# Kernel tuning notes

Measured on AMD Instinct MI355X. Metric: run time of the kernel, lower is better.

The kernel has to match this reference:

```python
import jax, jax.numpy as jnp
import numpy as np

D_MODEL = 1024
NUM_HEADS = 16
DK = D_MODEL // NUM_HEADS
THETA = 10000.0
B, S = 4, 2048


def _rope(x, pos):
    # x: [B, H, S, dk], pos: [S] int positions
    half = DK // 2
    inv_freq = THETA ** (-jnp.arange(half, dtype=jnp.float32) * 2.0 / DK)  # [half]
    ang = pos.astype(jnp.float32)[:, None] * inv_freq[None, :]             # [S, half]
    cos, sin = jnp.cos(ang), jnp.sin(ang)                                  # [S, half]
    x_even = x[..., 0::2]
    x_odd = x[..., 1::2]
    out_even = x_even * cos - x_odd * sin
    out_odd = x_even * sin + x_odd * cos
    # interleave back to [..., dk]
    return jnp.stack([out_even, out_odd], axis=-1).reshape(x.shape)


def setup_inputs() -> dict:
    key = jax.random.key(0)
    ks = jax.random.split(key, 5)
    scale = 1.0 / np.sqrt(D_MODEL)
    return {
        "x": jax.random.normal(ks[0], (B, S, D_MODEL), dtype=jnp.float32),
        "token_position": jnp.arange(S, dtype=jnp.int32),
        "wq": jax.random.normal(ks[1], (D_MODEL, D_MODEL), dtype=jnp.float32) * scale,
        "wk": jax.random.normal(ks[2], (D_MODEL, D_MODEL), dtype=jnp.float32) * scale,
        "wv": jax.random.normal(ks[3], (D_MODEL, D_MODEL), dtype=jnp.float32) * scale,
        "wo": jax.random.normal(ks[4], (D_MODEL, D_MODEL), dtype=jnp.float32) * scale,
    }


def reference(x, token_position, wq, wk, wv, wo):
    b, s, _ = x.shape
    # QKV projections (torch Linear: y = x @ W.T), split heads -> [B, H, S, dk]
    def proj(w):
        y = jnp.einsum("bsd,ed->bse", x, w)
        return y.reshape(b, s, NUM_HEADS, DK).transpose(0, 2, 1, 3)
    q, k, v = proj(wq), proj(wk), proj(wv)
    q = _rope(q, token_position)
    k = _rope(k, token_position)
    # causal SDPA
    scores = jnp.einsum("bhqd,bhkd->bhqk", q, k) / jnp.sqrt(jnp.float32(DK))
    causal = jnp.tril(jnp.ones((s, s), dtype=bool))
    scores = jnp.where(causal, scores, -jnp.inf)
    attn = jax.nn.softmax(scores, axis=-1)
    out = jnp.einsum("bhqk,bhkd->bhqd", attn, v)          # [B, H, S, dv]
    out = out.transpose(0, 2, 1, 3).reshape(b, s, D_MODEL)  # merge heads
    return jnp.einsum("bsd,ed->bse", out, wo)             # output projection
```

## Files before the change

### kernel.cpp

```cpp
#include <hip/hip_runtime.h>


#define D_MODEL 1024
#define NH      16
#define DKH     64
#define SEQ     2048
#define BATCH   4
#define M_ROWS  (BATCH * SEQ)
#define SCALE_LOG2 0.180336875461f
#define ROPE_L2    0.41524101186092029f

typedef _Float16 f16;
typedef _Float16 f16x8 __attribute__((ext_vector_type(8)));
typedef _Float16 f16x4 __attribute__((ext_vector_type(4)));
typedef _Float16 f16x2 __attribute__((ext_vector_type(2)));
typedef __fp16   fp16x2n __attribute__((ext_vector_type(2)));
typedef float    f32x4 __attribute__((ext_vector_type(4)));
typedef unsigned short u16;
typedef unsigned int   u32;

__device__ __forceinline__ void glds16(const void* g, void* l) {
  __builtin_amdgcn_global_load_lds((const __attribute__((address_space(1))) void*)g,
                                   (__attribute__((address_space(3))) void*)l, 16, 0, 0);
}
__device__ __forceinline__ u32 pk(float a, float b) {
  union { fp16x2n h; u32 u; } c; c.h = __builtin_amdgcn_cvt_pkrtz(a, b); return c.u;
}

__global__ void cvt_all(const float* __restrict__ x,
                        const float* __restrict__ w0, const float* __restrict__ w1,
                        const float* __restrict__ w2, const float* __restrict__ w3,
                        f16* __restrict__ xo, f16* __restrict__ o0, f16* __restrict__ o1,
                        f16* __restrict__ o2, f16* __restrict__ o3) {
  int blk = blockIdx.x;
  const float* src; f16* dst; int off;
  if (blk < 8192) { src = x; dst = xo; off = blk; }
  else {
    int t = blk - 8192; int w = t >> 10; off = t & 1023;
    switch (w) { case 0: src = w0; dst = o0; break;  case 1: src = w1; dst = o1; break;
                 case 2: src = w2; dst = o2; break;  default: src = w3; dst = o3; break; }
  }
  int i = (off * 256 + threadIdx.x) * 4;
  float4 v = *(const float4*)(src + i);
  uint2 o; o.x = pk(v.x, v.y); o.y = pk(v.z, v.w);
  *(uint2*)(dst + i) = o;
}

template<int MODE>
__global__ __launch_bounds__(256) void gemm_glds(const f16* __restrict__ A,
                                                 const f16* __restrict__ W,
                                                 void* __restrict__ C0,
                                                 void* __restrict__ C1,
                                                 void* __restrict__ C2,
                                                 const int* __restrict__ pos,
                                                 int K) {
  __shared__ f16 As[128][64];
  __shared__ f16 Bs[128][64];
  const int tid  = threadIdx.x;
  const int m0   = blockIdx.y * 128;
  const int n0   = blockIdx.x * 128;
  const int wave = tid >> 6, lane = tid & 63;
  const int quad = lane >> 4, l16 = lane & 15;
  const int wm = (wave >> 1) * 64, wn = (wave & 1) * 64;

  f32x4 acc[4][4];
#pragma unroll
  for (int i = 0; i < 4; ++i)
#pragma unroll
    for (int j = 0; j < 4; ++j) acc[i][j] = (f32x4){0.f, 0.f, 0.f, 0.f};

  for (int k0 = 0; k0 < K; k0 += 64) {
    if (k0) __syncthreads();
#pragma unroll
    for (int i = 0; i < 4; ++i) {
      int ci  = i * 256 + tid;
      int row = ci >> 3, ch = ci & 7;
      glds16(A + (size_t)(m0 + row) * K + k0 + ch * 8,
             (char*)&As[0][0] + (size_t)(i * 256 + (tid & 192)) * 16);
      glds16(W + (size_t)(n0 + row) * K + k0 + ch * 8,
             (char*)&Bs[0][0] + (size_t)(i * 256 + (tid & 192)) * 16);
    }
    __syncthreads();
#pragma unroll
    for (int kk = 0; kk < 64; kk += 32) {
      f16x8 af[4], bfr[4];
#pragma unroll
      for (int mi = 0; mi < 4; ++mi)
        af[mi] = *(const f16x8*)&As[wm + mi * 16 + l16][kk + quad * 8];
#pragma unroll
      for (int ni = 0; ni < 4; ++ni)
        bfr[ni] = *(const f16x8*)&Bs[wn + ni * 16 + l16][kk + quad * 8];
#pragma unroll
      for (int mi = 0; mi < 4; ++mi)
#pragma unroll
        for (int ni = 0; ni < 4; ++ni)
          acc[mi][ni] = __builtin_amdgcn_mfma_f32_16x16x32_f16(af[mi], bfr[ni], acc[mi][ni], 0, 0, 0);
    }
  }

  if (MODE == 1) {
    f16* dst; int nb;
    if (n0 < 1024)      { dst = (f16*)C0; nb = n0; }
    else if (n0 < 2048) { dst = (f16*)C1; nb = n0 - 1024; }
    else                { dst = (f16*)C2; nb = n0 - 2048; }
    if (n0 < 2048) {
      float invf[4], sgn[4];
#pragma unroll
      for (int ni = 0; ni < 4; ++ni) {
        int dk = (wn + ni * 16 + l16) & 63;
        invf[ni] = __builtin_amdgcn_exp2f(-ROPE_L2 * (float)(dk >> 1));
        sgn[ni]  = (dk & 1) ? 1.f : -1.f;
      }
#pragma unroll
      for (int mi = 0; mi < 4; ++mi)
#pragma unroll
        for (int r = 0; r < 4; ++r) {
          int row = m0 + wm + mi * 16 + quad * 4 + r;
          float ps = (float)pos[row & (SEQ - 1)];
#pragma unroll
          for (int ni = 0; ni < 4; ++ni) {
            float ang = ps * invf[ni];
            float c = __cosf(ang), sn = __sinf(ang);
            float v = acc[mi][ni][r];
            float p = __shfl_xor(v, 1);
            float ov = fmaf(p * sgn[ni], sn, v * c);
            int col = nb + wn + ni * 16 + l16;
            dst[(size_t)row * 1024 + col] = (f16)ov;
          }
        }
    } else {
#pragma unroll
      for (int mi = 0; mi < 4; ++mi)
#pragma unroll
        for (int ni = 0; ni < 4; ++ni)
#pragma unroll
          for (int r = 0; r < 4; ++r) {
            int row = m0 + wm + mi * 16 + quad * 4 + r;
            int col = nb + wn + ni * 16 + l16;
            dst[(size_t)row * 1024 + col] = (f16)acc[mi][ni][r];
          }
    }
  } else {
    float* dst = (float*)C0;
#pragma unroll
    for (int mi = 0; mi < 4; ++mi)
#pragma unroll
      for (int ni = 0; ni < 4; ++ni)
#pragma unroll
        for (int r = 0; r < 4; ++r) {
          int row = m0 + wm + mi * 16 + quad * 4 + r;
          int col = n0 + wn + ni * 16 + l16;
          dst[(size_t)row * 1024 + col] = acc[mi][ni][r];
        }
  }
}

__global__ __launch_bounds__(256, 3) void flash_attn(const f16* __restrict__ Q,
                                                     const f16* __restrict__ Kg,
                                                     const f16* __restrict__ Vg,
                                                     f16* __restrict__ O) {
  __shared__ char smem[38400];
  f16*  KsL         = (f16*)smem;
  u32   (*Vt)[67]   = (u32(*)[67])(smem + 16384);
  float (*Red0)[66] = (float(*)[66])smem;
  float (*Red1)[66] = (float(*)[66])(smem + 16896);
  float (*Lb)[17]   = (float(*)[17])(smem + 33792);

  const int tid  = threadIdx.x;
  const int bh   = blockIdx.x;
  const int b    = bh >> 4, h = bh & 15;
  const int qblk = 31 - (int)blockIdx.y;
  const int q0   = qblk * 64;
  const int wave = tid >> 6, lane = tid & 63;
  const int quad = lane >> 4, l16 = lane & 15;
  const int nkt  = (qblk + 2) >> 1;

  f16x8 qf[4][2];
#pragma unroll
  for (int nt = 0; nt < 4; ++nt)
#pragma unroll
    for (int ks = 0; ks < 2; ++ks) {
      f16x8 qv = *(const f16x8*)(Q + ((size_t)(b * SEQ + q0 + nt * 16 + l16)) * D_MODEL
                                   + h * DKH + ks * 32 + quad * 8);
      qf[nt][ks] = qv * (f16)SCALE_LOG2;
    }

  f32x4 o[4][4];
#pragma unroll
  for (int md = 0; md < 4; ++md)
#pragma unroll
    for (int nt = 0; nt < 4; ++nt) o[md][nt] = (f32x4){0.f, 0.f, 0.f, 0.f};
  float lacc[4] = {0.f, 0.f, 0.f, 0.f};

  const int kp = tid >> 3, dc = (tid & 7) * 8;

  for (int t = 0; t < nkt; ++t) {
    const int kt = t * 128;
    const f16* vb = Vg + ((size_t)(b * SEQ + kt + 2 * kp)) * D_MODEL + h * DKH + dc;
    uint4 v0 = *(const uint4*)vb;
    uint4 v1 = *(const uint4*)(vb + D_MODEL);
    uint4 v2 = *(const uint4*)(vb + 64 * D_MODEL);
    uint4 v3 = *(const uint4*)(vb + 65 * D_MODEL);

    if (t) __syncthreads();
#pragma unroll
    for (int i = 0; i < 4; ++i) {
      int ci = i * 256 + tid;
      int row = ci >> 3, gc = (ci & 7) ^ (row & 7);
      glds16(Kg + ((size_t)(b * SEQ + kt + row)) * D_MODEL + h * DKH + gc * 8,
             smem + (size_t)(i * 256 + (tid & 192)) * 16);
    }
    {
      union { uint4 u; u16 s[8]; } a0, a1, a2, a3;
      a0.u = v0; a1.u = v1; a2.u = v2; a3.u = v3;
#pragma unroll
      for (int j = 0; j < 8; ++j) {
        Vt[dc + j][kp]      = (u32)a0.s[j] | ((u32)a1.s[j] << 16);
        Vt[dc + j][32 + kp] = (u32)a2.s[j] | ((u32)a3.s[j] << 16);
      }
    }
    __syncthreads();

    f16x4 pb[2][4];
#pragma unroll
    for (int mt = 0; mt < 2; ++mt) {
      const int krow = wave * 32 + mt * 16 + l16;
      const int s0 = quad ^ (krow & 7);
      f16x8 ka0 = *(const f16x8*)(KsL + krow * 64 + s0 * 8);
      f16x8 ka1 = *(const f16x8*)(KsL + krow * 64 + (s0 ^ 4) * 8);
      const int keyb = kt + wave * 32 + mt * 16 + quad * 4;
#pragma unroll
      for (int nt = 0; nt < 4; ++nt) {
        f32x4 c = (f32x4){0.f, 0.f, 0.f, 0.f};
        c = __builtin_amdgcn_mfma_f32_16x16x32_f16(ka0, qf[nt][0], c, 0, 0, 0);
        c = __builtin_amdgcn_mfma_f32_16x16x32_f16(ka1, qf[nt][1], c, 0, 0, 0);
        const int q = q0 + nt * 16 + l16;
        float p0 = __builtin_amdgcn_exp2f(c[0]);
        float p1 = __builtin_amdgcn_exp2f(c[1]);
        float p2 = __builtin_amdgcn_exp2f(c[2]);
        float p3 = __builtin_amdgcn_exp2f(c[3]);
        if (t == nkt - 1) {
          p0 = (keyb + 0 <= q) ? p0 : 0.f;
          p1 = (keyb + 1 <= q) ? p1 : 0.f;
          p2 = (keyb + 2 <= q) ? p2 : 0.f;
          p3 = (keyb + 3 <= q) ? p3 : 0.f;
        }
        lacc[nt] += (p0 + p1) + (p2 + p3);
        union { u32 w[2]; f16x4 v; } pp;
        pp.w[0] = pk(p0, p1); pp.w[1] = pk(p2, p3);
        pb[mt][nt] = pp.v;
      }
    }

#pragma unroll
    for (int md = 0; md < 4; ++md)
#pragma unroll
      for (int ks2 = 0; ks2 < 2; ++ks2) {
        const u32* vp = &Vt[md * 16 + l16][wave * 16 + ks2 * 8 + quad * 2];
        union { u32 x[2]; f16x4 v; } va;
        va.x[0] = vp[0]; va.x[1] = vp[1];
#pragma unroll
        for (int nt = 0; nt < 4; ++nt)
          o[md][nt] = __builtin_amdgcn_mfma_f32_16x16x16f16(va.v, pb[ks2][nt], o[md][nt], 0, 0, 0);
      }
  }

  __syncthreads();
  {
    float (*Rw)[66] = (wave >= 2) ? Red1 : Red0;
    if ((wave & 1) == 0) {
#pragma unroll
      for (int md = 0; md < 4; ++md)
#pragma unroll
        for (int nt = 0; nt < 4; ++nt)
#pragma unroll
          for (int r = 0; r < 4; ++r)
            Rw[md * 16 + quad * 4 + r][nt * 16 + l16] = o[md][nt][r];
    }
#pragma unroll
    for (int nt = 0; nt < 4; ++nt)
      Lb[nt * 16 + l16][wave * 4 + quad] = lacc[nt];
    __syncthreads();
    if (wave & 1) {
#pragma unroll
      for (int md = 0; md < 4; ++md)
#pragma unroll
        for (int nt = 0; nt < 4; ++nt)
#pragma unroll
          for (int r = 0; r < 4; ++r)
            Rw[md * 16 + quad * 4 + r][nt * 16 + l16] += o[md][nt][r];
    }
    __syncthreads();
  }

  {
    const int q = tid & 63, dc4 = (tid >> 6) * 16;
    float lsum = 0.f;
#pragma unroll
    for (int j = 0; j < 16; ++j) lsum += Lb[q][j];
    float linv = __builtin_amdgcn_rcpf(lsum);
    union { uint4 u[2]; u32 w[8]; } ov;
#pragma unroll
    for (int i = 0; i < 8; ++i) {
      float f0 = Red0[dc4 + 2 * i][q]     + Red1[dc4 + 2 * i][q];
      float f1 = Red0[dc4 + 2 * i + 1][q] + Red1[dc4 + 2 * i + 1][q];
      ov.w[i] = pk(f0 * linv, f1 * linv);
    }
    f16* op = O + ((size_t)(b * SEQ + q0 + q)) * D_MODEL + h * DKH + dc4;
    *(uint4*)op = ov.u[0];
    *(uint4*)(op + 8) = ov.u[1];
  }
}

extern "C" void kernel_launch(void* const* d_in, const int* in_sizes, int n_in,
                              void* d_out, int out_size, void* d_ws, size_t ws_size,
                              hipStream_t stream) {
  const float* x      = (const float*)d_in[0];
  const int*   tokpos = (const int*)d_in[1];
  const float* wq     = (const float*)d_in[2];
  const float* wk     = (const float*)d_in[3];
  const float* wv     = (const float*)d_in[4];
  const float* wo     = (const float*)d_in[5];
  float* out = (float*)d_out;

  char* ws = (char*)d_ws;
  f16* Xb  = (f16*)(ws + 0);
  f16* Wqb = (f16*)(ws + 16777216);
  f16* Wkb = (f16*)(ws + 18874368);
  f16* Wvb = (f16*)(ws + 20971520);
  f16* Wob = (f16*)(ws + 23068672);
  f16* Qb  = (f16*)(ws + 25165824);
  f16* Kb  = (f16*)(ws + 41943040);
  f16* Vb  = (f16*)(ws + 58720256);
  f16* Ob  = Xb;

  cvt_all<<<12288, 256, 0, stream>>>(x, wq, wk, wv, wo, Xb, Wqb, Wkb, Wvb, Wob);

  gemm_glds<1><<<dim3(24, 64), 256, 0, stream>>>(Xb, Wqb, Qb, Kb, Vb, tokpos, D_MODEL);

  flash_attn<<<dim3(BATCH * NH, 32), 256, 0, stream>>>(Qb, Kb, Vb, Ob);

  gemm_glds<0><<<dim3(8, 64), 256, 0, stream>>>(Ob, Wob, out, nullptr, nullptr, nullptr, D_MODEL);
}
```

Measured before the change: 255.9 us.

## Double-buffer GEMM with 8-wave 128x256 tiles and swizzled LDS

Replaces the single-buffered 128x128 GEMM with a 512-thread, 128x256-tile kernel. It double-buffers half-K slabs in dynamic LDS using async global-to-LDS loads and explicit vmcnt waits. It also XOR-swizzles the LDS layout to avoid bank conflicts and raises MFMA priority with setprio. The aim is to overlap global loads with MFMA work and improve operand reuse. The cost is 96KB of LDS per block and fewer blocks in the grid, which may limit occupancy and load balance on the small output projection GEMM.

```diff
diff --git a/kernel.cpp b/kernel.cpp
--- a/kernel.cpp
+++ b/kernel.cpp
@@ -13,7 +13,6 @@
 typedef _Float16 f16;
 typedef _Float16 f16x8 __attribute__((ext_vector_type(8)));
 typedef _Float16 f16x4 __attribute__((ext_vector_type(4)));
-typedef _Float16 f16x2 __attribute__((ext_vector_type(2)));
 typedef __fp16   fp16x2n __attribute__((ext_vector_type(2)));
 typedef float    f32x4 __attribute__((ext_vector_type(4)));
 typedef unsigned short u16;
@@ -46,22 +45,32 @@
   *(uint2*)(dst + i) = o;
 }
 
+__device__ __forceinline__ void mfma16(f32x4 (&acc)[4][4], const f16x8 (&af)[4],
+                                       const f16x8 (&bf)[4]) {
+#pragma unroll
+  for (int mi = 0; mi < 4; ++mi)
+#pragma unroll
+    for (int ni = 0; ni < 4; ++ni)
+      acc[mi][ni] = __builtin_amdgcn_mfma_f32_16x16x32_f16(af[mi], bf[ni], acc[mi][ni], 0, 0, 0);
+}
+
 template<int MODE>
-__global__ __launch_bounds__(256) void gemm_glds(const f16* __restrict__ A,
+__global__ __launch_bounds__(512, 2) void gemm8p(const f16* __restrict__ A,
                                                  const f16* __restrict__ W,
                                                  void* __restrict__ C0,
                                                  void* __restrict__ C1,
                                                  void* __restrict__ C2,
                                                  const int* __restrict__ pos,
                                                  int K) {
-  __shared__ f16 As[128][64];
-  __shared__ f16 Bs[128][64];
+  extern __shared__ char lds[];
   const int tid  = threadIdx.x;
   const int m0   = blockIdx.y * 128;
-  const int n0   = blockIdx.x * 128;
+  const int n0   = blockIdx.x * 256;
   const int wave = tid >> 6, lane = tid & 63;
   const int quad = lane >> 4, l16 = lane & 15;
-  const int wm = (wave >> 1) * 64, wn = (wave & 1) * 64;
+  const int wm = (wave >> 2) * 64;
+  const int wn = (wave & 3) * 64;
+  const int nt = K >> 6;
 
   f32x4 acc[4][4];
 #pragma unroll
@@ -69,32 +78,75 @@
 #pragma unroll
     for (int j = 0; j < 4; ++j) acc[i][j] = (f32x4){0.f, 0.f, 0.f, 0.f};
 
-  for (int k0 = 0; k0 < K; k0 += 64) {
-    if (k0) __syncthreads();
-#pragma unroll
-    for (int i = 0; i < 4; ++i) {
-      int ci  = i * 256 + tid;
-      int row = ci >> 3, ch = ci & 7;
-      glds16(A + (size_t)(m0 + row) * K + k0 + ch * 8,
-             (char*)&As[0][0] + (size_t)(i * 256 + (tid & 192)) * 16);
-      glds16(W + (size_t)(n0 + row) * K + k0 + ch * 8,
-             (char*)&Bs[0][0] + (size_t)(i * 256 + (tid & 192)) * 16);
-    }
-    __syncthreads();
-#pragma unroll
-    for (int kk = 0; kk < 64; kk += 32) {
-      f16x8 af[4], bfr[4];
-#pragma unroll
-      for (int mi = 0; mi < 4; ++mi)
-        af[mi] = *(const f16x8*)&As[wm + mi * 16 + l16][kk + quad * 8];
-#pragma unroll
-      for (int ni = 0; ni < 4; ++ni)
-        bfr[ni] = *(const f16x8*)&Bs[wn + ni * 16 + l16][kk + quad * 8];
-#pragma unroll
-      for (int mi = 0; mi < 4; ++mi)
-#pragma unroll
-        for (int ni = 0; ni < 4; ++ni)
-          acc[mi][ni] = __builtin_amdgcn_mfma_f32_16x16x32_f16(af[mi], bfr[ni], acc[mi][ni], 0, 0, 0);
+  auto stageA = [&](int t, int h) {
+    char* dst = lds + ((t & 1) * 16384 + h * 8192) + (size_t)(tid & 448) * 16;
+    int r = tid >> 2, c = tid & 3;
+    int g = c ^ ((r >> 1) & 3);
+    glds16(A + (size_t)(m0 + r) * K + (t * 64 + h * 32) + g * 8, dst);
+  };
+  auto stageB = [&](int t, int h) {
+    char* base = lds + 32768 + ((t & 1) * 32768 + h * 16384);
+#pragma unroll
+    for (int j = 0; j < 2; ++j) {
+      int ci = j * 512 + tid;
+      int r = ci >> 2, c = ci & 3;
+      int g = c ^ ((r >> 1) & 3);
+      glds16(W + (size_t)(n0 + r) * K + (t * 64 + h * 32) + g * 8,
+             base + (size_t)(j * 512 + (tid & 448)) * 16);
+    }
+  };
+  auto readA = [&](int t, int h, int mi) -> f16x8 {
+    int r = wm + mi * 16 + l16;
+    int c = quad ^ ((r >> 1) & 3);
+    return *(const f16x8*)(lds + (t & 1) * 16384 + h * 8192 + r * 64 + c * 16);
+  };
+  auto readB = [&](int t, int h, int ni) -> f16x8 {
+    int r = wn + ni * 16 + l16;
+    int c = quad ^ ((r >> 1) & 3);
+    return *(const f16x8*)(lds + 32768 + (t & 1) * 32768 + h * 16384 + r * 64 + c * 16);
+  };
+
+  stageA(0, 0); stageB(0, 0);
+  stageA(0, 1); stageB(0, 1);
+  stageA(1, 0); stageB(1, 0);
+  asm volatile("s_waitcnt vmcnt(6)" ::: "memory");
+  __builtin_amdgcn_sched_barrier(0);
+  __builtin_amdgcn_s_barrier();
+
+  for (int t = 0; t < nt; ++t) {
+    {
+      f16x8 af[4], bf[4];
+#pragma unroll
+      for (int i = 0; i < 4; ++i) { af[i] = readA(t, 0, i); bf[i] = readB(t, 0, i); }
+      if (t + 1 < nt) { stageA(t + 1, 1); stageB(t + 1, 1); }
+      __builtin_amdgcn_s_barrier();
+      asm volatile("s_waitcnt lgkmcnt(0)" ::: "memory");
+      __builtin_amdgcn_sched_barrier(0);
+      __builtin_amdgcn_s_setprio(1);
+      mfma16(acc, af, bf);
+      __builtin_amdgcn_s_setprio(0);
+      if (t < nt - 1) asm volatile("s_waitcnt vmcnt(6)" ::: "memory");
+      else            asm volatile("s_waitcnt vmcnt(0)" ::: "memory");
+      __builtin_amdgcn_sched_barrier(0);
+      __builtin_amdgcn_s_barrier();
+    }
+    {
+      f16x8 af[4], bf[4];
+#pragma unroll
+      for (int i = 0; i < 4; ++i) { af[i] = readA(t, 1, i); bf[i] = readB(t, 1, i); }
+      if (t + 2 < nt) { stageA(t + 2, 0); stageB(t + 2, 0); }
+      __builtin_amdgcn_s_barrier();
+      asm volatile("s_waitcnt lgkmcnt(0)" ::: "memory");
+      __builtin_amdgcn_sched_barrier(0);
+      __builtin_amdgcn_s_setprio(1);
+      mfma16(acc, af, bf);
+      __builtin_amdgcn_s_setprio(0);
+      if (t < nt - 1) {
+        if (t < nt - 2) asm volatile("s_waitcnt vmcnt(6)" ::: "memory");
+        else            asm volatile("s_waitcnt vmcnt(3)" ::: "memory");
+        __builtin_amdgcn_sched_barrier(0);
+        __builtin_amdgcn_s_barrier();
+      }
     }
   }
 
@@ -334,11 +386,22 @@
   f16* Vb  = (f16*)(ws + 58720256);
   f16* Ob  = Xb;
 
+  static bool attr_done = false;
+  if (!attr_done) {
+    auto* f1 = gemm8p<1>;
+    auto* f0 = gemm8p<0>;
+    (void)hipFuncSetAttribute(reinterpret_cast<const void*>(f1),
+                              hipFuncAttributeMaxDynamicSharedMemorySize, 98304);
+    (void)hipFuncSetAttribute(reinterpret_cast<const void*>(f0),
+                              hipFuncAttributeMaxDynamicSharedMemorySize, 98304);
+    attr_done = true;
+  }
+
   cvt_all<<<12288, 256, 0, stream>>>(x, wq, wk, wv, wo, Xb, Wqb, Wkb, Wvb, Wob);
 
-  gemm_glds<1><<<dim3(24, 64), 256, 0, stream>>>(Xb, Wqb, Qb, Kb, Vb, tokpos, D_MODEL);
+  gemm8p<1><<<dim3(12, 64), 512, 98304, stream>>>(Xb, Wqb, Qb, Kb, Vb, tokpos, D_MODEL);
 
   flash_attn<<<dim3(BATCH * NH, 32), 256, 0, stream>>>(Qb, Kb, Vb, Ob);
 
-  gemm_glds<0><<<dim3(8, 64), 256, 0, stream>>>(Ob, Wob, out, nullptr, nullptr, nullptr, D_MODEL);
-}
+  gemm8p<0><<<dim3(4, 64), 512, 98304, stream>>>(Ob, Wob, out, nullptr, nullptr, nullptr, D_MODEL);
+}
```

Measured after the change: 265.4 us. 1.04x slower.

## Rewrite projection GEMMs as 8-wave 128x256 tiles with triple-buffered LDS pipeline

Applied to the files above, without the earlier changes.

Replaces the 4-wave 128x128 GEMM with a 512-thread kernel that computes 128x256 tiles. It uses three LDS stages in 147KB of dynamic shared memory, with XOR-swizzled LDS addressing and global-to-LDS loads issued one stage ahead of the MFMA work. It also uses explicit vmcnt waits, barriers and setprio around the MFMA block to overlap memory traffic with compute. The aim is to hide global load latency and cut LDS bank conflicts in the QKV and output projections. The cost is higher LDS use, which limits occupancy to one block per CU, and a K loop hard-wired to 1024.

```diff
diff --git a/kernel.cpp b/kernel.cpp
--- a/kernel.cpp
+++ b/kernel.cpp
@@ -13,7 +13,6 @@
 typedef _Float16 f16;
 typedef _Float16 f16x8 __attribute__((ext_vector_type(8)));
 typedef _Float16 f16x4 __attribute__((ext_vector_type(4)));
-typedef _Float16 f16x2 __attribute__((ext_vector_type(2)));
 typedef __fp16   fp16x2n __attribute__((ext_vector_type(2)));
 typedef float    f32x4 __attribute__((ext_vector_type(4)));
 typedef unsigned short u16;
@@ -47,21 +46,20 @@
 }
 
 template<int MODE>
-__global__ __launch_bounds__(256) void gemm_glds(const f16* __restrict__ A,
+__global__ __launch_bounds__(512, 2) void gemm8p(const f16* __restrict__ A,
                                                  const f16* __restrict__ W,
                                                  void* __restrict__ C0,
                                                  void* __restrict__ C1,
                                                  void* __restrict__ C2,
-                                                 const int* __restrict__ pos,
-                                                 int K) {
-  __shared__ f16 As[128][64];
-  __shared__ f16 Bs[128][64];
+                                                 const int* __restrict__ pos) {
+  extern __shared__ char lds[];
   const int tid  = threadIdx.x;
   const int m0   = blockIdx.y * 128;
-  const int n0   = blockIdx.x * 128;
+  const int n0   = blockIdx.x * 256;
   const int wave = tid >> 6, lane = tid & 63;
   const int quad = lane >> 4, l16 = lane & 15;
-  const int wm = (wave >> 1) * 64, wn = (wave & 1) * 64;
+  const int wm = (wave >> 2) * 64;
+  const int wn = (wave & 3) * 64;
 
   f32x4 acc[4][4];
 #pragma unroll
@@ -69,34 +67,80 @@
 #pragma unroll
     for (int j = 0; j < 4; ++j) acc[i][j] = (f32x4){0.f, 0.f, 0.f, 0.f};
 
-  for (int k0 = 0; k0 < K; k0 += 64) {
-    if (k0) __syncthreads();
-#pragma unroll
-    for (int i = 0; i < 4; ++i) {
-      int ci  = i * 256 + tid;
-      int row = ci >> 3, ch = ci & 7;
-      glds16(A + (size_t)(m0 + row) * K + k0 + ch * 8,
-             (char*)&As[0][0] + (size_t)(i * 256 + (tid & 192)) * 16);
-      glds16(W + (size_t)(n0 + row) * K + k0 + ch * 8,
-             (char*)&Bs[0][0] + (size_t)(i * 256 + (tid & 192)) * 16);
-    }
-    __syncthreads();
-#pragma unroll
-    for (int kk = 0; kk < 64; kk += 32) {
-      f16x8 af[4], bfr[4];
-#pragma unroll
-      for (int mi = 0; mi < 4; ++mi)
-        af[mi] = *(const f16x8*)&As[wm + mi * 16 + l16][kk + quad * 8];
-#pragma unroll
-      for (int ni = 0; ni < 4; ++ni)
-        bfr[ni] = *(const f16x8*)&Bs[wn + ni * 16 + l16][kk + quad * 8];
-#pragma unroll
-      for (int mi = 0; mi < 4; ++mi)
-#pragma unroll
-        for (int ni = 0; ni < 4; ++ni)
-          acc[mi][ni] = __builtin_amdgcn_mfma_f32_16x16x32_f16(af[mi], bfr[ni], acc[mi][ni], 0, 0, 0);
-    }
-  }
+  const int cswr = (quad ^ ((l16 >> 1) & 3)) * 16;
+  const char* aB  = lds + (wm + l16) * 64 + cswr;
+  const char* bB0 = lds + 49152 + (wn + l16) * 64 + cswr;
+  const char* bB1 = bB0 + 49152;
+
+  const int sr = tid >> 2;
+  const int sg = (tid & 3) ^ ((sr >> 1) & 3);
+  const char* pA = (const char*)(A + (size_t)(m0 + sr) * 1024 + sg * 8);
+  const char* pB = (const char*)(W + (size_t)(n0 + sr) * 1024 + sg * 8);
+  char* const sA = lds + (size_t)(tid & 448) * 16;
+  char* const sB = lds + 49152 + (size_t)(tid & 448) * 16;
+
+#define STAGE(SBUF) do {                                                      \
+    glds16(pA,                sA + (SBUF) * 16384);                           \
+    glds16(pA + 64,           sA + (SBUF) * 16384 + 8192);                    \
+    glds16(pB,                sB + (SBUF) * 16384);                           \
+    glds16(pB + 262144,       sB + (SBUF) * 16384 + 8192);                    \
+    glds16(pB + 64,           sB + (SBUF) * 16384 + 49152);                   \
+    glds16(pB + 262144 + 64,  sB + (SBUF) * 16384 + 49152 + 8192);            \
+    pA += 128; pB += 128;                                                     \
+  } while (0)
+
+#define GPHASE(BUF, SBUF, DOSTAGE, VMN, LASTP) do {                           \
+    f16x8 af[4][2], bf[4][2];                                                 \
+    _Pragma("unroll")                                                         \
+    for (int mi = 0; mi < 4; ++mi) {                                          \
+      af[mi][0] = *(const f16x8*)(aB + ((BUF) * 16384 + mi * 1024));          \
+      af[mi][1] = *(const f16x8*)(aB + ((BUF) * 16384 + 8192 + mi * 1024));   \
+    }                                                                         \
+    _Pragma("unroll")                                                         \
+    for (int ni = 0; ni < 4; ++ni) {                                          \
+      bf[ni][0] = *(const f16x8*)(bB0 + ((BUF) * 16384 + ni * 1024));         \
+      bf[ni][1] = *(const f16x8*)(bB1 + ((BUF) * 16384 + ni * 1024));         \
+    }                                                                         \
+    if (DOSTAGE) STAGE(SBUF);                                                 \
+    __builtin_amdgcn_s_barrier();                                             \
+    asm volatile("s_waitcnt lgkmcnt(0)" ::: "memory");                        \
+    __builtin_amdgcn_sched_barrier(0);                                        \
+    __builtin_amdgcn_s_setprio(1);                                            \
+    _Pragma("unroll")                                                         \
+    for (int h = 0; h < 2; ++h)                                               \
+      _Pragma("unroll")                                                       \
+      for (int mi = 0; mi < 4; ++mi)                                          \
+        _Pragma("unroll")                                                     \
+        for (int ni = 0; ni < 4; ++ni)                                        \
+          acc[mi][ni] = __builtin_amdgcn_mfma_f32_16x16x32_f16(af[mi][h], bf[ni][h], \
+                                                               acc[mi][ni], 0, 0, 0); \
+    __builtin_amdgcn_s_setprio(0);                                            \
+    if (!(LASTP)) {                                                           \
+      asm volatile("s_waitcnt vmcnt(" #VMN ")" ::: "memory");                 \
+      __builtin_amdgcn_sched_barrier(0);                                      \
+      __builtin_amdgcn_s_barrier();                                           \
+    }                                                                         \
+  } while (0)
+
+  STAGE(0);
+  STAGE(1);
+  asm volatile("s_waitcnt vmcnt(6)" ::: "memory");
+  __builtin_amdgcn_sched_barrier(0);
+  __builtin_amdgcn_s_barrier();
+
+#pragma unroll 1
+  for (int it = 0; it < 4; ++it) {
+    GPHASE(0, 2, 1, 6, 0);
+    GPHASE(1, 0, 1, 6, 0);
+    GPHASE(2, 1, 1, 6, 0);
+  }
+  GPHASE(0, 2, 1, 6, 0);
+  GPHASE(1, 0, 1, 6, 0);
+  GPHASE(2, 0, 0, 0, 0);
+  GPHASE(0, 0, 0, 0, 1);
+
+#undef GPHASE
+#undef STAGE
 
   if (MODE == 1) {
     f16* dst; int nb;
@@ -334,11 +378,22 @@
   f16* Vb  = (f16*)(ws + 58720256);
   f16* Ob  = Xb;
 
+  static bool attr_done = false;
+  if (!attr_done) {
+    auto* f1 = gemm8p<1>;
+    auto* f0 = gemm8p<0>;
+    (void)hipFuncSetAttribute(reinterpret_cast<const void*>(f1),
+                              hipFuncAttributeMaxDynamicSharedMemorySize, 147456);
+    (void)hipFuncSetAttribute(reinterpret_cast<const void*>(f0),
+                              hipFuncAttributeMaxDynamicSharedMemorySize, 147456);
+    attr_done = true;
+  }
+
   cvt_all<<<12288, 256, 0, stream>>>(x, wq, wk, wv, wo, Xb, Wqb, Wkb, Wvb, Wob);
 
-  gemm_glds<1><<<dim3(24, 64), 256, 0, stream>>>(Xb, Wqb, Qb, Kb, Vb, tokpos, D_MODEL);
+  gemm8p<1><<<dim3(12, 64), 512, 147456, stream>>>(Xb, Wqb, Qb, Kb, Vb, tokpos);
 
   flash_attn<<<dim3(BATCH * NH, 32), 256, 0, stream>>>(Qb, Kb, Vb, Ob);
 
-  gemm_glds<0><<<dim3(8, 64), 256, 0, stream>>>(Ob, Wob, out, nullptr, nullptr, nullptr, D_MODEL);
-}
+  gemm8p<0><<<dim3(4, 64), 512, 147456, stream>>>(Ob, Wob, out, nullptr, nullptr, nullptr);
+}
```

Result: no change. 252.5 us (-1.3%).

## Replace GEMMs with 256x256-tile double-buffered pipelined kernel with XCD-aware block mapping

Applied to the files above, without the earlier changes.

Swaps the 128x128 single-buffered GEMM for a 512-thread, 256x256-tile kernel that double-buffers A/B tiles in 128KB of dynamic LDS. Each k-step is split into half-tile stages that interleave async global->LDS loads with MFMA, using explicit vmcnt waits, barriers and setprio. It also adds a swizzled LDS layout to cut bank conflicts and remaps block IDs so neighbouring tiles share an XCD. The aim is to hide load latency and raise arithmetic intensity. The risks are fewer blocks (only 128 for the output projection), fragile hand scheduling, and hardcoded K=1024.

```diff
diff --git a/kernel.cpp b/kernel.cpp
--- a/kernel.cpp
+++ b/kernel.cpp
@@ -6,14 +6,12 @@
 #define DKH     64
 #define SEQ     2048
 #define BATCH   4
-#define M_ROWS  (BATCH * SEQ)
 #define SCALE_LOG2 0.180336875461f
 #define ROPE_L2    0.41524101186092029f
 
 typedef _Float16 f16;
 typedef _Float16 f16x8 __attribute__((ext_vector_type(8)));
 typedef _Float16 f16x4 __attribute__((ext_vector_type(4)));
-typedef _Float16 f16x2 __attribute__((ext_vector_type(2)));
 typedef __fp16   fp16x2n __attribute__((ext_vector_type(2)));
 typedef float    f32x4 __attribute__((ext_vector_type(4)));
 typedef unsigned short u16;
@@ -46,111 +44,177 @@
   *(uint2*)(dst + i) = o;
 }
 
-template<int MODE>
-__global__ __launch_bounds__(256) void gemm_glds(const f16* __restrict__ A,
-                                                 const f16* __restrict__ W,
-                                                 void* __restrict__ C0,
-                                                 void* __restrict__ C1,
-                                                 void* __restrict__ C2,
-                                                 const int* __restrict__ pos,
-                                                 int K) {
-  __shared__ f16 As[128][64];
-  __shared__ f16 Bs[128][64];
+#define VMW_(N) asm volatile("s_waitcnt vmcnt(" #N ")" ::: "memory")
+#define VMW(N) VMW_(N)
+
+template<int MODE, int CPX, int NBX>
+__global__ __launch_bounds__(512, 2) void gemm256(const f16* __restrict__ A,
+                                                  const f16* __restrict__ W,
+                                                  void* __restrict__ C0,
+                                                  void* __restrict__ C1,
+                                                  void* __restrict__ C2,
+                                                  const int* __restrict__ pos) {
+  extern __shared__ char lds[];
+  const int bid  = blockIdx.x;
+  const int lin  = (bid & 7) * CPX + (bid >> 3);
+  const int bx   = lin % NBX, by = lin / NBX;
+  const int m0   = by * 256, n0 = bx * 256;
   const int tid  = threadIdx.x;
-  const int m0   = blockIdx.y * 128;
-  const int n0   = blockIdx.x * 128;
   const int wave = tid >> 6, lane = tid & 63;
   const int quad = lane >> 4, l16 = lane & 15;
-  const int wm = (wave >> 1) * 64, wn = (wave & 1) * 64;
-
-  f32x4 acc[4][4];
-#pragma unroll
-  for (int i = 0; i < 4; ++i)
+  const int wr   = wave >> 2, wc = wave & 3;
+
+  f32x4 acc[8][4];
+#pragma unroll
+  for (int i = 0; i < 8; ++i)
 #pragma unroll
     for (int j = 0; j < 4; ++j) acc[i][j] = (f32x4){0.f, 0.f, 0.f, 0.f};
 
-  for (int k0 = 0; k0 < K; k0 += 64) {
-    if (k0) __syncthreads();
-#pragma unroll
-    for (int i = 0; i < 4; ++i) {
-      int ci  = i * 256 + tid;
-      int row = ci >> 3, ch = ci & 7;
-      glds16(A + (size_t)(m0 + row) * K + k0 + ch * 8,
-             (char*)&As[0][0] + (size_t)(i * 256 + (tid & 192)) * 16);
-      glds16(W + (size_t)(n0 + row) * K + k0 + ch * 8,
-             (char*)&Bs[0][0] + (size_t)(i * 256 + (tid & 192)) * 16);
-    }
-    __syncthreads();
-#pragma unroll
-    for (int kk = 0; kk < 64; kk += 32) {
-      f16x8 af[4], bfr[4];
-#pragma unroll
-      for (int mi = 0; mi < 4; ++mi)
-        af[mi] = *(const f16x8*)&As[wm + mi * 16 + l16][kk + quad * 8];
-#pragma unroll
-      for (int ni = 0; ni < 4; ++ni)
-        bfr[ni] = *(const f16x8*)&Bs[wn + ni * 16 + l16][kk + quad * 8];
-#pragma unroll
-      for (int mi = 0; mi < 4; ++mi)
-#pragma unroll
-        for (int ni = 0; ni < 4; ++ni)
-          acc[mi][ni] = __builtin_amdgcn_mfma_f32_16x16x32_f16(af[mi], bfr[ni], acc[mi][ni], 0, 0, 0);
-    }
-  }
+  const int posR = (l16 & 1) * 4 + (quad ^ ((l16 >> 1) & 3));
+  const char* aRd = lds + wr * 8192 + (l16 >> 1) * 128 + posR * 16;
+  const char* bRd = lds + 65536 + wc * 4096 + (l16 >> 1) * 128 + posR * 16;
+
+  const int r0 = 2 * (tid >> 3) + ((tid & 7) >> 2);
+  const int c0 = (tid & 3) ^ ((tid >> 3) & 3);
+  const f16* pA0 = A + (size_t)(m0 + r0) * 1024 + c0 * 8;
+  const f16* pA1 = pA0 + (size_t)128 * 1024;
+  const f16* pB0 = W + (size_t)(n0 + r0) * 1024 + c0 * 8;
+  const f16* pB1 = pB0 + (size_t)128 * 1024;
+  char* const sdA = lds + (size_t)(tid & 448) * 16;
+  char* const sdB = lds + 65536 + (size_t)(tid & 448) * 16;
+
+#define ST_A(TB, H) do {                                                      \
+    glds16(pA0 + (H) * 32, sdA + (TB) * 32768 + (H) * 16384);                 \
+    glds16(pA1 + (H) * 32, sdA + (TB) * 32768 + (H) * 16384 + 8192);          \
+  } while (0)
+#define ST_B(TB, H) do {                                                      \
+    glds16(pB0 + (H) * 32, sdB + (TB) * 32768 + (H) * 16384);                 \
+    glds16(pB1 + (H) * 32, sdB + (TB) * 32768 + (H) * 16384 + 8192);          \
+  } while (0)
+#define RDA(BUF, H, MG) do { _Pragma("unroll")                                \
+    for (int i_ = 0; i_ < 4; ++i_)                                            \
+      af[i_] = *(const f16x8*)(aRd + (BUF) * 32768 + (H) * 16384 +            \
+                               (MG) * 4096 + i_ * 1024);                      \
+  } while (0)
+#define RDB(BUF, H) do { _Pragma("unroll")                                    \
+    for (int j_ = 0; j_ < 4; ++j_)                                            \
+      bf[j_] = *(const f16x8*)(bRd + (BUF) * 32768 + (H) * 16384 + j_ * 1024);\
+  } while (0)
+#define MM(MG) do { _Pragma("unroll")                                         \
+    for (int i_ = 0; i_ < 4; ++i_) { _Pragma("unroll")                        \
+      for (int j_ = 0; j_ < 4; ++j_)                                          \
+        acc[(MG) * 4 + i_][j_] = __builtin_amdgcn_mfma_f32_16x16x32_f16(      \
+            af[i_], bf[j_], acc[(MG) * 4 + i_][j_], 0, 0, 0); }               \
+  } while (0)
+#define PRE_MFMA() do {                                                       \
+    __builtin_amdgcn_s_barrier();                                             \
+    asm volatile("s_waitcnt lgkmcnt(0)" ::: "memory");                        \
+    __builtin_amdgcn_sched_barrier(0);                                        \
+  } while (0)
+
+#define TILE(BUF, DOSTAGE, VM2, VM4, LAST) do {                               \
+    f16x8 af[4], bf[4];                                                       \
+    RDA(BUF, 0, 0); RDB(BUF, 0);                                              \
+    if (DOSTAGE) ST_A((BUF) ^ 1, 0);                                          \
+    PRE_MFMA();                                                               \
+    __builtin_amdgcn_s_setprio(1); MM(0); __builtin_amdgcn_s_setprio(0);      \
+    __builtin_amdgcn_s_barrier();                                             \
+    RDA(BUF, 0, 1);                                                           \
+    if (DOSTAGE) ST_B((BUF) ^ 1, 0);                                          \
+    PRE_MFMA();                                                               \
+    __builtin_amdgcn_s_setprio(1); MM(1); __builtin_amdgcn_s_setprio(0);      \
+    VMW(VM2); __builtin_amdgcn_sched_barrier(0);                              \
+    __builtin_amdgcn_s_barrier();                                             \
+    RDA(BUF, 1, 0); RDB(BUF, 1);                                              \
+    if (DOSTAGE) ST_A((BUF) ^ 1, 1);                                          \
+    PRE_MFMA();                                                               \
+    __builtin_amdgcn_s_setprio(1); MM(0); __builtin_amdgcn_s_setprio(0);      \
+    __builtin_amdgcn_s_barrier();                                             \
+    RDA(BUF, 1, 1);                                                           \
+    if (DOSTAGE) ST_B((BUF) ^ 1, 1);                                          \
+    PRE_MFMA();                                                               \
+    __builtin_amdgcn_s_setprio(1); MM(1); __builtin_amdgcn_s_setprio(0);      \
+    if (!(LAST)) {                                                            \
+      VMW(VM4); __builtin_amdgcn_sched_barrier(0);                            \
+      __builtin_amdgcn_s_barrier();                                           \
+    }                                                                         \
+    if (DOSTAGE) { pA0 += 64; pA1 += 64; pB0 += 64; pB1 += 64; }              \
+  } while (0)
+
+  ST_A(0, 0); ST_B(0, 0); ST_A(0, 1); ST_B(0, 1);
+  pA0 += 64; pA1 += 64; pB0 += 64; pB1 += 64;
+  VMW(4); __builtin_amdgcn_sched_barrier(0);
+  __builtin_amdgcn_s_barrier();
+
+#pragma unroll 1
+  for (int it = 0; it < 7; ++it) {
+    TILE(0, 1, 4, 4, 0);
+    TILE(1, 1, 4, 4, 0);
+  }
+  TILE(0, 1, 4, 4, 0);
+  TILE(1, 0, 0, 0, 1);
+
+#undef TILE
+#undef PRE_MFMA
+#undef MM
+#undef RDB
+#undef RDA
+#undef ST_B
+#undef ST_A
 
   if (MODE == 1) {
     f16* dst; int nb;
-    if (n0 < 1024)      { dst = (f16*)C0; nb = n0; }
-    else if (n0 < 2048) { dst = (f16*)C1; nb = n0 - 1024; }
-    else                { dst = (f16*)C2; nb = n0 - 2048; }
-    if (n0 < 2048) {
+    if (bx < 4)      { dst = (f16*)C0; nb = n0; }
+    else if (bx < 8) { dst = (f16*)C1; nb = n0 - 1024; }
+    else             { dst = (f16*)C2; nb = n0 - 2048; }
+    if (bx < 8) {
       float invf[4], sgn[4];
 #pragma unroll
       for (int ni = 0; ni < 4; ++ni) {
-        int dk = (wn + ni * 16 + l16) & 63;
+        int dk = (wc * 64 + ni * 16 + l16) & 63;
         invf[ni] = __builtin_amdgcn_exp2f(-ROPE_L2 * (float)(dk >> 1));
         sgn[ni]  = (dk & 1) ? 1.f : -1.f;
       }
 #pragma unroll
-      for (int mi = 0; mi < 4; ++mi)
+      for (int a = 0; a < 8; ++a)
 #pragma unroll
         for (int r = 0; r < 4; ++r) {
-          int row = m0 + wm + mi * 16 + quad * 4 + r;
+          int row = m0 + wr * 128 + a * 16 + quad * 4 + r;
           float ps = (float)pos[row & (SEQ - 1)];
 #pragma unroll
           for (int ni = 0; ni < 4; ++ni) {
             float ang = ps * invf[ni];
             float c = __cosf(ang), sn = __sinf(ang);
-            float v = acc[mi][ni][r];
+            float v = acc[a][ni][r];
             float p = __shfl_xor(v, 1);
             float ov = fmaf(p * sgn[ni], sn, v * c);
-            int col = nb + wn + ni * 16 + l16;
+            int col = nb + wc * 64 + ni * 16 + l16;
             dst[(size_t)row * 1024 + col] = (f16)ov;
           }
         }
     } else {
 #pragma unroll
-      for (int mi = 0; mi < 4; ++mi)
+      for (int a = 0; a < 8; ++a)
 #pragma unroll
         for (int ni = 0; ni < 4; ++ni)
 #pragma unroll
           for (int r = 0; r < 4; ++r) {
-            int row = m0 + wm + mi * 16 + quad * 4 + r;
-            int col = nb + wn + ni * 16 + l16;
-            dst[(size_t)row * 1024 + col] = (f16)acc[mi][ni][r];
+            int row = m0 + wr * 128 + a * 16 + quad * 4 + r;
+            int col = nb + wc * 64 + ni * 16 + l16;
+            dst[(size_t)row * 1024 + col] = (f16)acc[a][ni][r];
           }
     }
   } else {
     float* dst = (float*)C0;
 #pragma unroll
-    for (int mi = 0; mi < 4; ++mi)
+    for (int a = 0; a < 8; ++a)
 #pragma unroll
       for (int ni = 0; ni < 4; ++ni)
 #pragma unroll
         for (int r = 0; r < 4; ++r) {
-          int row = m0 + wm + mi * 16 + quad * 4 + r;
-          int col = n0 + wn + ni * 16 + l16;
-          dst[(size_t)row * 1024 + col] = acc[mi][ni][r];
+          int row = m0 + wr * 128 + a * 16 + quad * 4 + r;
+          int col = n0 + wc * 64 + ni * 16 + l16;
+          dst[(size_t)row * 1024 + col] = acc[a][ni][r];
         }
   }
 }
@@ -334,11 +398,22 @@
   f16* Vb  = (f16*)(ws + 58720256);
   f16* Ob  = Xb;
 
+  static bool attr_done = false;
+  if (!attr_done) {
+    auto* f1 = gemm256<1, 48, 12>;
+    auto* f0 = gemm256<0, 16, 4>;
+    (void)hipFuncSetAttribute(reinterpret_cast<const void*>(f1),
+                              hipFuncAttributeMaxDynamicSharedMemorySize, 131072);
+    (void)hipFuncSetAttribute(reinterpret_cast<const void*>(f0),
+                              hipFuncAttributeMaxDynamicSharedMemorySize, 131072);
+    attr_done = true;
+  }
+
   cvt_all<<<12288, 256, 0, stream>>>(x, wq, wk, wv, wo, Xb, Wqb, Wkb, Wvb, Wob);
 
-  gemm_glds<1><<<dim3(24, 64), 256, 0, stream>>>(Xb, Wqb, Qb, Kb, Vb, tokpos, D_MODEL);
+  gemm256<1, 48, 12><<<384, 512, 131072, stream>>>(Xb, Wqb, Qb, Kb, Vb, tokpos);
 
   flash_attn<<<dim3(BATCH * NH, 32), 256, 0, stream>>>(Qb, Kb, Vb, Ob);
 
-  gemm_glds<0><<<dim3(8, 64), 256, 0, stream>>>(Ob, Wob, out, nullptr, nullptr, nullptr, D_MODEL);
-}
+  gemm256<0, 16, 4><<<128, 512, 131072, stream>>>(Ob, Wob, out, nullptr, nullptr, tokpos);
+}
```

After: 259.2 us. About the same (+1.3%).
